# Kernel optimization log

Measured on AMD Instinct MI355X. Metric: run time of the kernel, lower is better.

## Reference

```python
import jax, jax.numpy as jnp
import numpy as np

B, D, N = 128, 2, 8192
C_CENT, K, R = 32, 32, 0.25
BOTTLE = 8
BN_EPS = 1e-5


def setup_inputs() -> dict:
    key = jax.random.key(0)
    ks = jax.random.split(key, 12)
    w = lambda k, s: jax.random.normal(k, s, dtype=jnp.float32) * 0.05
    z = lambda s: jnp.zeros(s, jnp.float32)
    o = lambda s: jnp.ones(s, jnp.float32)
    return {
        "x": jax.random.normal(ks[0], (B, D, N), dtype=jnp.float32),
        "eps": jax.random.normal(ks[1], (B, BOTTLE), dtype=jnp.float32),
        "sa_c1_w": w(ks[2], (64, D)), "sa_c1_b": z((64,)),
        "sa_bn1_g": o((64,)), "sa_bn1_b": z((64,)),
        "sa_c2_w": w(ks[3], (128, 64)), "sa_c2_b": z((128,)),
        "sa_bn2_g": o((128,)), "sa_bn2_b": z((128,)),
        "sa_c3_w": w(ks[4], (256, 128)), "sa_c3_b": z((256,)),
        "sa_bn3_g": o((256,)), "sa_bn3_b": z((256,)),
        "sa_fc1_w": w(ks[5], (1024, 256 * C_CENT)), "sa_fc1_b": z((1024,)),
        "sa_bn4_g": o((1024,)), "sa_bn4_b": z((1024,)),
        "sa_fc2_w": w(ks[6], (256, 1024)), "sa_fc2_b": z((256,)),
        "sa_bn5_g": o((256,)), "sa_bn5_b": z((256,)),
        "sa_fc3_w": w(ks[7], (BOTTLE, 256)), "sa_fc3_b": z((BOTTLE,)),
        "fce1_w": w(ks[8], (BOTTLE, BOTTLE)), "fce1_b": z((BOTTLE,)),
        "fce2_w": w(ks[9], (BOTTLE, BOTTLE)), "fce2_b": z((BOTTLE,)),
        "dfc1_w": w(ks[10], (32, BOTTLE)), "dfc1_b": z((32,)),
        "dfc2_w": w(ks[11], (128, 32)), "dfc2_b": z((128,)),
        "dfc3_w": w(jax.random.fold_in(key, 99), (512, 128)), "dfc3_b": z((512,)),
    }


def _bn2d(x, g, b):
    m = jnp.mean(x, axis=(0, 2, 3), keepdims=True)
    v = jnp.var(x, axis=(0, 2, 3), keepdims=True)
    return (x - m) * jax.lax.rsqrt(v + BN_EPS) * g[None, :, None, None] + b[None, :, None, None]


def _bn1d(x, g, b):
    m = jnp.mean(x, axis=0, keepdims=True)
    v = jnp.var(x, axis=0, keepdims=True)
    return (x - m) * jax.lax.rsqrt(v + BN_EPS) * g[None, :] + b[None, :]


def _fps(points, n_centroids):
    # points: [B, D, N]; deterministic start at index 0 (torch uses randint)
    c0 = points[:, :, 0]                                   # [B, D]
    dist0 = jnp.sum((c0[:, :, None] - points) ** 2, axis=1)  # [B, N]

    def step(dist, _):
        ind = jnp.argmax(dist, axis=1)                      # [B]
        c = jnp.take_along_axis(points, ind[:, None, None], axis=2)[:, :, 0]  # [B, D]
        dist = jnp.minimum(dist, jnp.sum((c[:, :, None] - points) ** 2, axis=1))
        return dist, c

    _, cs = jax.lax.scan(step, dist0, None, length=n_centroids - 1)  # [C-1, B, D]
    cents = jnp.concatenate([c0[None], cs], axis=0)          # [C, B, D]
    return jnp.transpose(cents, (1, 2, 0))                   # [B, D, C]


def _group_points(points):
    b, _, n = points.shape
    cents = _fps(points, C_CENT)                             # [B, D, C]
    # squared pairwise distances centroid->point: [B, C, N]
    sq = (-2.0 * jnp.einsum('bdc,bdn->bcn', cents, points)
          + jnp.sum(cents ** 2, axis=1)[:, :, None]
          + jnp.sum(points ** 2, axis=1)[:, None, :])
    idx = jnp.broadcast_to(jnp.arange(n, dtype=jnp.int32), (b, C_CENT, n))
    idx = jnp.where(sq > R * R, jnp.int32(n), idx)
    idx = jnp.sort(idx, axis=-1)[:, :, :K]                   # [B, C, K]
    first = idx[:, :, :1]
    idx = jnp.where(idx == n, first, idx)
    bidx = jnp.arange(b)[:, None, None]
    grouped = points[bidx, :, idx]                            # [B, C, K, D]
    return jnp.transpose(grouped, (0, 3, 1, 2))               # [B, D, C, K]


def reference(x, eps, sa_c1_w, sa_c1_b, sa_bn1_g, sa_bn1_b, sa_c2_w, sa_c2_b,
              sa_bn2_g, sa_bn2_b, sa_c3_w, sa_c3_b, sa_bn3_g, sa_bn3_b,
              sa_fc1_w, sa_fc1_b, sa_bn4_g, sa_bn4_b, sa_fc2_w, sa_fc2_b,
              sa_bn5_g, sa_bn5_b, sa_fc3_w, sa_fc3_b, fce1_w, fce1_b,
              fce2_w, fce2_b, dfc1_w, dfc1_b, dfc2_w, dfc2_b, dfc3_w, dfc3_b):
    b = x.shape[0]
    g = _group_points(x)                                     # [B, D, C, K]
    h = jax.nn.relu(_bn2d(jnp.einsum('bdck,od->bock', g, sa_c1_w) + sa_c1_b[None, :, None, None], sa_bn1_g, sa_bn1_b))
    h = jax.nn.relu(_bn2d(jnp.einsum('bdck,od->bock', h, sa_c2_w) + sa_c2_b[None, :, None, None], sa_bn2_g, sa_bn2_b))
    h = jax.nn.relu(_bn2d(jnp.einsum('bdck,od->bock', h, sa_c3_w) + sa_c3_b[None, :, None, None], sa_bn3_g, sa_bn3_b))
    h = jnp.max(h, axis=3)                                   # [B, 256, C]
    h = h.reshape(b, 256 * C_CENT)
    h = jax.nn.relu(_bn1d(h @ sa_fc1_w.T + sa_fc1_b, sa_bn4_g, sa_bn4_b))
    h = jax.nn.relu(_bn1d(h @ sa_fc2_w.T + sa_fc2_b, sa_bn5_g, sa_bn5_b))
    feat = jax.nn.relu(h @ sa_fc3_w.T + sa_fc3_b)            # [B, 8]
    mu = feat @ fce1_w.T + fce1_b
    logvar = feat @ fce2_w.T + fce2_b
    zlat = eps * jnp.exp(0.5 * logvar) + mu                  # reparametrize
    d = jax.nn.relu(zlat @ dfc1_w.T + dfc1_b)
    d = jax.nn.relu(d @ dfc2_w.T + dfc2_b)
    d = d @ dfc3_w.T + dfc3_b
    out = d.reshape(-1, 2, 256)
    return out, mu, logvar
```

## Files before the change

### kernel.cpp

```cpp
#include <hip/hip_runtime.h>
#include <cstdint>
#include <cstddef>

#define NB   128
#define NPT  8192
#define NC   32
#define NK   32
#define MSP  131072
#define R2   0.0625f

typedef unsigned short u16;
typedef unsigned long long u64;
typedef __attribute__((ext_vector_type(8))) short short8v;
typedef __attribute__((ext_vector_type(4))) float f32x4;

static constexpr size_t OFF_CENTS  = 0;
static constexpr size_t OFF_GX     = 8192;
static constexpr size_t OFF_GY     = OFF_GX + 131072;
static constexpr size_t OFF_H1Q    = OFF_GY + 131072;
static constexpr size_t OFF_H2Q    = OFF_H1Q + 4194304;
static constexpr size_t OFF_MAXPRE = OFF_H1Q;
static constexpr size_t OFF_P3S    = OFF_H1Q + 1048576;
static constexpr size_t OFF_P3Q    = OFF_H1Q + 2097152;
static constexpr size_t OFF_PART1  = OFF_H2Q;
static constexpr size_t OFF_PART2  = OFF_H2Q + 4194304;
static constexpr size_t OFF_FC1    = OFF_H2Q + 8388608;
static constexpr size_t OFF_FC2    = OFF_FC1 + 131072;
static constexpr size_t OFF_W2Q    = OFF_FC2 + 32768;
static constexpr size_t OFF_W3Q    = OFF_W2Q + 4096;
static constexpr size_t OFF_PMOM   = OFF_W3Q + 16384;
static constexpr size_t OFF_P2S    = OFF_PMOM + 20480;
static constexpr size_t OFF_P2Q    = OFF_P2S + 131072;
static constexpr size_t OFF_SC1    = OFF_P2Q + 131072;
static constexpr size_t OFF_SH1    = OFF_SC1 + 64;
static constexpr size_t OFF_SC2    = OFF_SH1 + 64;
static constexpr size_t OFF_SH2    = OFF_SC2 + 128;
static constexpr size_t OFF_SC3    = OFF_SH2 + 128;
static constexpr size_t OFF_SH3    = OFF_SC3 + 256;
static constexpr size_t OFF_SC4    = OFF_SH3 + 256;
static constexpr size_t OFF_SH4    = OFF_SC4 + 1024;
static constexpr size_t OFF_SC5    = OFF_SH4 + 1024;
static constexpr size_t OFF_SH5    = OFF_SC5 + 256;
static constexpr size_t OFF_SC3E   = OFF_SH5 + 256;
static constexpr size_t OFF_SH3E   = OFF_SC3E + 8192;

__device__ __forceinline__ u16 f2bf(float f) {
  uint32_t u = __float_as_uint(f);
  u += 0x7FFFu + ((u >> 16) & 1u);
  return (u16)(u >> 16);
}
__device__ __forceinline__ float bf2f(u16 h) {
  return __uint_as_float(((uint32_t)h) << 16);
}
__device__ __forceinline__ void gload16(const void* g, void* l) {
  __builtin_amdgcn_global_load_lds(
      (const __attribute__((address_space(1))) void*)g,
      (__attribute__((address_space(3))) void*)l, 16, 0, 0);
}

__global__ __launch_bounds__(512) void fps_kernel(const float* __restrict__ x,
                                                  float* __restrict__ cents,
                                                  const float* __restrict__ c2w,
                                                  const float* __restrict__ c3w,
                                                  u16* __restrict__ w2q,
                                                  u16* __restrict__ w3qf) {
  const int b = blockIdx.x, t = threadIdx.x;
  const int lane = t & 63, wid = t >> 6;

  if (b < 12) {
    const int id = b * 512 + t;
    if (id < 2048) {
      const int e = id * 4;
      const float4 v = *(const float4*)(c2w + e);
      uint2 q;
      q.x = (uint32_t)f2bf(v.x) | ((uint32_t)f2bf(v.y) << 16);
      q.y = (uint32_t)f2bf(v.z) | ((uint32_t)f2bf(v.w) << 16);
      *(uint2*)(w2q + e) = q;
    } else {
      const int id2 = id - 2048;
      const int oc = id2 >> 4, k8 = (id2 & 15) * 8;
      const float4 v0 = *(const float4*)(c3w + oc * 128 + k8);
      const float4 v1 = *(const float4*)(c3w + oc * 128 + k8 + 4);
      uint4 q;
      q.x = (uint32_t)f2bf(v0.x) | ((uint32_t)f2bf(v0.y) << 16);
      q.y = (uint32_t)f2bf(v0.z) | ((uint32_t)f2bf(v0.w) << 16);
      q.z = (uint32_t)f2bf(v1.x) | ((uint32_t)f2bf(v1.y) << 16);
      q.w = (uint32_t)f2bf(v1.z) | ((uint32_t)f2bf(v1.w) << 16);
      const int off = ((((oc >> 4) * 4 + (k8 >> 5)) * 4 + ((k8 & 31) >> 3)) * 16 + (oc & 15)) * 8;
      *(uint4*)(w3qf + off) = q;
    }
  }

  const float* xb = x + (size_t)b * 2 * NPT;
  float px[16], py[16], dst[16];
  __shared__ float lpx[NPT], lpy[NPT];
  __shared__ u64 slot[2][8];
  __shared__ float cxs[NC], cys[NC];
#pragma unroll
  for (int k = 0; k < 16; k++) {
    const int id = t + k * 512;
    px[k] = xb[id];
    py[k] = xb[NPT + id];
    lpx[id] = px[k];
    lpy[id] = py[k];
  }
  const float c0x = xb[0], c0y = xb[NPT];
  if (t == 0) { cxs[0] = c0x; cys[0] = c0y; }
  float bm = -1.0f;
  int bi = 0;
#pragma unroll
  for (int k = 0; k < 16; k++) {
    const float dx = __fsub_rn(c0x, px[k]);
    const float dy = __fsub_rn(c0y, py[k]);
    dst[k] = __fadd_rn(__fmul_rn(dx, dx), __fmul_rn(dy, dy));
    if (dst[k] > bm) { bm = dst[k]; bi = t + k * 512; }
  }
  u64 best = ((u64)__float_as_uint(bm) << 32) | (uint32_t)~(uint32_t)bi;
  __syncthreads();
  for (int j = 1; j < NC; j++) {
#pragma unroll
    for (int off = 1; off < 64; off <<= 1) {
      const u64 o = __shfl_xor(best, off);
      if (o > best) best = o;
    }
    const int pb = j & 1;
    if (lane == 0) slot[pb][wid] = best;
    __syncthreads();
    u64 w = slot[pb][0];
#pragma unroll
    for (int s = 1; s < 8; s++) {
      const u64 o = slot[pb][s];
      if (o > w) w = o;
    }
    const int wi = (int)~(uint32_t)w;
    const float wx = lpx[wi], wy = lpy[wi];
    if (t == 0) { cxs[j] = wx; cys[j] = wy; }
    bm = -1.0f;
    bi = 0;
#pragma unroll
    for (int k = 0; k < 16; k++) {
      const float dx = __fsub_rn(wx, px[k]);
      const float dy = __fsub_rn(wy, py[k]);
      const float nd = __fadd_rn(__fmul_rn(dx, dx), __fmul_rn(dy, dy));
      dst[k] = fminf(dst[k], nd);
      if (dst[k] > bm) { bm = dst[k]; bi = t + k * 512; }
    }
    best = ((u64)__float_as_uint(bm) << 32) | (uint32_t)~(uint32_t)bi;
  }
  __syncthreads();
  if (t < NC) {
    cents[(size_t)b * 64 + t]      = cxs[t];
    cents[(size_t)b * 64 + 32 + t] = cys[t];
  }
}

__global__ __launch_bounds__(512) void group_kernel(const float* __restrict__ x,
                                                    const float* __restrict__ cents,
                                                    float* __restrict__ gx,
                                                    float* __restrict__ gy,
                                                    float* __restrict__ pmom) {
  const int b  = blockIdx.x & 127;
  const int cg = blockIdx.x >> 7;
  const int t = threadIdx.x;
  const int lane = t & 63, wid = t >> 6;
  const float* px = x + (size_t)b * 2 * NPT;
  const float* py = px + NPT;
  const int p0 = t * 16;

  float lx[16], ly[16], sp[16];
#pragma unroll
  for (int k = 0; k < 16; k += 4) {
    const float4 vx = *(const float4*)(px + p0 + k);
    const float4 vy = *(const float4*)(py + p0 + k);
    lx[k] = vx.x; lx[k + 1] = vx.y; lx[k + 2] = vx.z; lx[k + 3] = vx.w;
    ly[k] = vy.x; ly[k + 1] = vy.y; ly[k + 2] = vy.z; ly[k + 3] = vy.w;
  }
#pragma unroll
  for (int k = 0; k < 16; k++)
    sp[k] = __fadd_rn(__fmul_rn(lx[k], lx[k]), __fmul_rn(ly[k], ly[k]));

  __shared__ int idxs[8][NK];
  __shared__ int wtot[8][8];
  uint32_t mask[8];
  int ebase[8];

#pragma unroll
  for (int c = 0; c < 8; c++) {
    const int cc = cg * 8 + c;
    const float cx = cents[(size_t)b * 64 + cc];
    const float cy = cents[(size_t)b * 64 + 32 + cc];
    const float sc = __fadd_rn(__fmul_rn(cx, cx), __fmul_rn(cy, cy));
    uint32_t m = 0;
#pragma unroll
    for (int k = 0; k < 16; k++) {
      const float dot = __fadd_rn(__fmul_rn(cx, lx[k]), __fmul_rn(cy, ly[k]));
      const float sq  = __fadd_rn(__fadd_rn(__fmul_rn(-2.0f, dot), sc), sp[k]);
      if (!(sq > R2)) m |= (1u << k);
    }
    mask[c] = m;
    const int cnt = (int)__popc(m);
    int pre = cnt;
#pragma unroll
    for (int off = 1; off < 64; off <<= 1) {
      const int o = __shfl_up(pre, off);
      if (lane >= off) pre += o;
    }
    ebase[c] = pre - cnt;
    if (lane == 63) wtot[c][wid] = pre;
  }
  __syncthreads();
#pragma unroll
  for (int c = 0; c < 8; c++) {
    int off = 0;
#pragma unroll
    for (int w = 0; w < 8; w++) off += (w < wid) ? wtot[c][w] : 0;
    int pos = ebase[c] + off;
    uint32_t m = mask[c];
    while (m && pos < NK) {
      const int k = __ffs(m) - 1;
      idxs[c][pos] = p0 + k;
      m &= m - 1;
      pos++;
    }
  }
  __syncthreads();
  {
    int tot = 0;
#pragma unroll
    for (int w = 0; w < 8; w++) tot += wtot[wid][w];
    if (lane >= tot && lane < NK) idxs[wid][lane] = idxs[wid][0];
  }
  __syncthreads();
  {
    const int bc = b * 32 + cg * 8 + wid;
    float gxv = 0.f, gyv = 0.f;
    if (lane < NK) {
      const int id = idxs[wid][lane];
      gxv = px[id];
      gyv = py[id];
      const size_t s = (size_t)bc * NK + lane;
      gx[s] = gxv;
      gy[s] = gyv;
    }
    float sx = gxv, sy = gyv;
    float sxx = gxv * gxv, syy = gyv * gyv, sxy = gxv * gyv;
#pragma unroll
    for (int off = 1; off < 64; off <<= 1) {
      sx  += __shfl_xor(sx, off);
      sy  += __shfl_xor(sy, off);
      sxx += __shfl_xor(sxx, off);
      syy += __shfl_xor(syy, off);
      sxy += __shfl_xor(sxy, off);
    }
    if (lane == 0) {
      pmom[0 * 4096 + bc] = sx;
      pmom[1 * 4096 + bc] = sy;
      pmom[2 * 4096 + bc] = sxx;
      pmom[3 * 4096 + bc] = syy;
      pmom[4 * 4096 + bc] = sxy;
    }
  }
}

__global__ __launch_bounds__(256) void bn1fin_kernel(const float* __restrict__ pmom,
                                                     const float* __restrict__ w,
                                                     const float* __restrict__ gamma,
                                                     const float* __restrict__ beta,
                                                     float* __restrict__ sc,
                                                     float* __restrict__ sh) {
  const int t = threadIdx.x, lane = t & 63, wid = t >> 6;
  __shared__ float rr[5][4];
  __shared__ float red[5];
#pragma unroll
  for (int m = 0; m < 5; m++) {
    float a = 0.f;
#pragma unroll
    for (int i = 0; i < 4; i++) {
      const float4 v = *(const float4*)(pmom + m * 4096 + (t + i * 256) * 4);
      a += v.x + v.y + v.z + v.w;
    }
#pragma unroll
    for (int off = 1; off < 64; off <<= 1) a += __shfl_xor(a, off);
    if (lane == 0) rr[m][wid] = a;
  }
  __syncthreads();
  if (t == 0) {
#pragma unroll
    for (int m = 0; m < 5; m++) red[m] = rr[m][0] + rr[m][1] + rr[m][2] + rr[m][3];
  }
  __syncthreads();
  if (t < 64) {
    const double invM = 1.0 / (double)MSP;
    const double mx = red[0] * invM, my = red[1] * invM;
    const double exx = red[2] * invM, eyy = red[3] * invM, exy = red[4] * invM;
    const double w0 = w[2 * t], w1 = w[2 * t + 1];
    const double mean = w0 * mx + w1 * my;
    double var = w0 * w0 * (exx - mx * mx) + 2.0 * w0 * w1 * (exy - mx * my)
               + w1 * w1 * (eyy - my * my);
    if (var < 0.0) var = 0.0;
    const double s = (double)gamma[t] / sqrt(var + 1e-5);
    sc[t] = (float)s;
    sh[t] = (float)((double)beta[t] - mean * s);
  }
}

__global__ __launch_bounds__(256) void finalize_kernel(
    const float* __restrict__ psum, const float* __restrict__ psq,
    int P, float invM,
    const float* __restrict__ gamma, const float* __restrict__ beta,
    float* __restrict__ scale, float* __restrict__ shift,
    float* __restrict__ scexp, float* __restrict__ shexp, int expand) {
  const int c = blockIdx.x, t = threadIdx.x;
  float s = 0.f, q = 0.f;
  for (int p = t; p < P; p += 256) {
    s += psum[(size_t)c * P + p];
    q += psq[(size_t)c * P + p];
  }
#pragma unroll
  for (int off = 1; off < 64; off <<= 1) {
    s += __shfl_xor(s, off);
    q += __shfl_xor(q, off);
  }
  __shared__ float r1[4], r2[4], bc2[2];
  if ((t & 63) == 0) { r1[t >> 6] = s; r2[t >> 6] = q; }
  __syncthreads();
  if (t == 0) {
    s = r1[0] + r1[1] + r1[2] + r1[3];
    q = r2[0] + r2[1] + r2[2] + r2[3];
    const float m = s * invM;
    float v = fmaf(-m, m, q * invM);
    v = fmaxf(v, 0.f);
    const float sc = gamma[c] * (float)(1.0 / sqrt((double)v + 1e-5));
    const float sh = fmaf(-m, sc, beta[c]);
    scale[c] = sc;
    shift[c] = sh;
    bc2[0] = sc;
    bc2[1] = sh;
  }
  __syncthreads();
  if (t < expand) {
    scexp[c * expand + t] = bc2[0];
    shexp[c * expand + t] = bc2[1];
  }
}

__global__ __launch_bounds__(256) void bncol_kernel(
    const float* __restrict__ in, int rows, int cols,
    const float* __restrict__ gamma, const float* __restrict__ beta,
    float* __restrict__ scale, float* __restrict__ shift) {
  const int jl = threadIdx.x & 63;
  const int rg = threadIdx.x >> 6;
  const int j = blockIdx.x * 64 + jl;
  float s = 0.f, q = 0.f;
  for (int r = rg; r < rows; r += 4) {
    const float v = in[(size_t)r * cols + j];
    s += v;
    q = fmaf(v, v, q);
  }
  __shared__ float rs[4][64], rq[4][64];
  rs[rg][jl] = s;
  rq[rg][jl] = q;
  __syncthreads();
  if (rg == 0) {
    s = rs[0][jl] + rs[1][jl] + rs[2][jl] + rs[3][jl];
    q = rq[0][jl] + rq[1][jl] + rq[2][jl] + rq[3][jl];
    const float m = s / (float)rows;
    float var = q / (float)rows - m * m;
    var = fmaxf(var, 0.f);
    const float sc = gamma[j] * (float)(1.0 / sqrt((double)var + 1e-5));
    scale[j] = sc;
    shift[j] = fmaf(-m, sc, beta[j]);
  }
}

__global__ __launch_bounds__(512) void conv2fused_kernel(
    const float* __restrict__ gx, const float* __restrict__ gy,
    const float* __restrict__ w1,
    const float* __restrict__ sc1, const float* __restrict__ sh1,
    const u16* __restrict__ wq,
    u16* __restrict__ outq,
    float* __restrict__ psum, float* __restrict__ psq) {
  constexpr int K = 64, OCB = 128, BS = 128, OCT = 128;
  constexpr int RB = K * 2;
  constexpr int STAGE = (OCB + BS) * RB;
  constexpr int EPI = BS * OCB * 2 + 4 * OCB * 2 * 4;
  constexpr int SMEM = STAGE > EPI ? STAGE : EPI;
  __shared__ __align__(16) char smem[SMEM + 1024];
  char* Wl = smem;
  char* Bl = smem + OCB * RB;
  float* par = (float*)(smem + SMEM);
  const int t = threadIdx.x;
  const int lane = t & 63, wid = t >> 6;
  const int sblk = blockIdx.x;
  const int s_base = sblk * BS;

  if (t < 64) {
    par[t]       = w1[t * 2];
    par[64 + t]  = w1[t * 2 + 1];
    par[128 + t] = sc1[t];
    par[192 + t] = sh1[t];
  }
  __syncthreads();

  {
    constexpr int CH = OCB * RB / 16, PW = CH / 8, NI = PW / 64;
#pragma unroll
    for (int j = 0; j < NI; j++) {
      const int c = wid * PW + j * 64 + lane;
      const int b = c * 16;
      const int oc = b / RB;
      const int off = b & (RB - 1);
      gload16((const char*)wq + (size_t)oc * RB + (off ^ ((oc & 7) << 4)),
              Wl + (wid * PW + j * 64) * 16);
    }
  }
  {
    const int sl = t >> 2;
    const int cq = t & 3;
    const float xx = gx[s_base + sl], yy = gy[s_base + sl];
    uint32_t pk[8];
#pragma unroll
    for (int h = 0; h < 8; h++) {
      const int c = cq * 16 + 2 * h;
      float v0 = fmaf(par[c],     xx, par[64 + c]     * yy);
      float v1 = fmaf(par[c + 1], xx, par[64 + c + 1] * yy);
      v0 = fmaxf(fmaf(v0, par[128 + c],     par[192 + c]),     0.f);
      v1 = fmaxf(fmaf(v1, par[128 + c + 1], par[192 + c + 1]), 0.f);
      pk[h] = (uint32_t)f2bf(v0) | ((uint32_t)f2bf(v1) << 16);
    }
    *(uint4*)(Bl + sl * RB + ((cq * 32)      ^ ((sl & 7) << 4))) = *(uint4*)&pk[0];
    *(uint4*)(Bl + sl * RB + ((cq * 32 + 16) ^ ((sl & 7) << 4))) = *(uint4*)&pk[4];
  }
  __syncthreads();

  const int wr = wid >> 2, wc = wid & 3;
  const int l15 = lane & 15, l4 = lane >> 4;
  f32x4 acc[4][2];
#pragma unroll
  for (int fo = 0; fo < 4; fo++)
#pragma unroll
    for (int fs = 0; fs < 2; fs++)
#pragma unroll
      for (int q = 0; q < 4; q++) acc[fo][fs][q] = 0.f;

#pragma unroll
  for (int ks = 0; ks < K / 32; ks++) {
    short8v a[4], bv[2];
#pragma unroll
    for (int f = 0; f < 4; f++) {
      const int oc = wr * 64 + f * 16 + l15;
      a[f] = *(const short8v*)(Wl + oc * RB + ((ks * 64 + l4 * 16) ^ ((oc & 7) << 4)));
    }
#pragma unroll
    for (int f = 0; f < 2; f++) {
      const int sl = wc * 32 + f * 16 + l15;
      bv[f] = *(const short8v*)(Bl + sl * RB + ((ks * 64 + l4 * 16) ^ ((sl & 7) << 4)));
    }
#pragma unroll
    for (int fo = 0; fo < 4; fo++)
#pragma unroll
      for (int fs = 0; fs < 2; fs++)
        acc[fo][fs] = __builtin_amdgcn_mfma_f32_16x16x32_bf16(a[fo], bv[fs], acc[fo][fs], 0, 0, 0);
  }
  __syncthreads();

  char* Dl = smem;
  float* sred1 = (float*)(smem + BS * OCB * 2);
  float* sred2 = sred1 + 4 * OCB;

#pragma unroll
  for (int fo = 0; fo < 4; fo++)
#pragma unroll
    for (int r = 0; r < 4; r++) {
      float s1 = acc[fo][0][r] + acc[fo][1][r];
      float s2 = fmaf(acc[fo][0][r], acc[fo][0][r], acc[fo][1][r] * acc[fo][1][r]);
#pragma unroll
      for (int off = 1; off < 16; off <<= 1) {
        s1 += __shfl_xor(s1, off);
        s2 += __shfl_xor(s2, off);
      }
      if (l15 == 0) {
        const int ocl = wr * 64 + fo * 16 + l4 * 4 + r;
        sred1[wc * OCB + ocl] = s1;
        sred2[wc * OCB + ocl] = s2;
      }
    }

#pragma unroll
  for (int fo = 0; fo < 4; fo++)
#pragma unroll
    for (int fs = 0; fs < 2; fs++) {
      const int sl = wc * 32 + fs * 16 + l15;
      const int ocl = wr * 64 + fo * 16 + l4 * 4;
      uint2 q;
      q.x = (uint32_t)f2bf(acc[fo][fs][0]) | ((uint32_t)f2bf(acc[fo][fs][1]) << 16);
      q.y = (uint32_t)f2bf(acc[fo][fs][2]) | ((uint32_t)f2bf(acc[fo][fs][3]) << 16);
      *(uint2*)(Dl + sl * 256 + ((ocl * 2) ^ ((sl & 7) << 4))) = q;
    }
  __syncthreads();

  if (t < OCB) {
    psum[(size_t)t * 1024 + sblk] =
        sred1[t] + sred1[OCB + t] + sred1[2 * OCB + t] + sred1[3 * OCB + t];
    psq[(size_t)t * 1024 + sblk] =
        sred2[t] + sred2[OCB + t] + sred2[2 * OCB + t] + sred2[3 * OCB + t];
  }
#pragma unroll
  for (int i = 0; i < 4; i++) {
    const int c = t + i * 512;
    const int sl = c >> 4, slot = c & 15;
    const uint4 v = *(const uint4*)(Dl + sl * 256 + ((slot * 16) ^ ((sl & 7) << 4)));
    *(uint4*)(outq + (size_t)(s_base + sl) * OCT + slot * 8) = v;
  }
}

__global__ __launch_bounds__(512) void conv3_kernel(
    const u16* __restrict__ act,
    const u16* __restrict__ wqf,
    const float* __restrict__ ascale, const float* __restrict__ ashift,
    float* __restrict__ psum, float* __restrict__ psq,
    float* __restrict__ maxpre) {
  constexpr int K = 128, RB = 256;
  __shared__ __align__(16) char Bl[64 * RB];
  const int t = threadIdx.x;
  const int lane = t & 63, wid = t >> 6;
  const int ws = wid & 1, wo = wid >> 1;
  const int sblk = blockIdx.x;
  const int l15 = lane & 15, l4 = lane >> 4;
  const int s_base = sblk * 64;

  short8v b[4][4];
  {
    const int ocq0 = wo * 4;
#pragma unroll
    for (int fo = 0; fo < 4; fo++)
#pragma unroll
      for (int ks = 0; ks < 4; ks++)
        b[fo][ks] = *(const short8v*)(wqf + ((((ocq0 + fo) * 4 + ks) * 4 + l4) * 16 + l15) * 8);
  }

  {
    const int kk0 = (t & 15) * 8;
    const float4 scA = *(const float4*)(ascale + kk0);
    const float4 scB = *(const float4*)(ascale + kk0 + 4);
    const float4 shA = *(const float4*)(ashift + kk0);
    const float4 shB = *(const float4*)(ashift + kk0 + 4);
    const float scr[8] = {scA.x, scA.y, scA.z, scA.w, scB.x, scB.y, scB.z, scB.w};
    const float shr[8] = {shA.x, shA.y, shA.z, shA.w, shB.x, shB.y, shB.z, shB.w};
#pragma unroll
    for (int i = 0; i < 2; i++) {
      const int sl = (t >> 4) + i * 32;
      const uint4 raw = *(const uint4*)(act + (size_t)(s_base + sl) * K + kk0);
      const u16* rp = (const u16*)&raw;
      uint32_t pk[4];
#pragma unroll
      for (int h = 0; h < 4; h++) {
        const float f0 = fmaxf(fmaf(bf2f(rp[2 * h]),     scr[2 * h],     shr[2 * h]),     0.f);
        const float f1 = fmaxf(fmaf(bf2f(rp[2 * h + 1]), scr[2 * h + 1], shr[2 * h + 1]), 0.f);
        pk[h] = (uint32_t)f2bf(f0) | ((uint32_t)f2bf(f1) << 16);
      }
      *(uint4*)(Bl + sl * RB + ((kk0 * 2) ^ ((sl & 7) << 4))) = *(uint4*)pk;
    }
  }
  __syncthreads();

  f32x4 acc[2][4];
#pragma unroll
  for (int fs = 0; fs < 2; fs++)
#pragma unroll
    for (int fo = 0; fo < 4; fo++)
#pragma unroll
      for (int q = 0; q < 4; q++) acc[fs][fo][q] = 0.f;

#pragma unroll
  for (int ks = 0; ks < 4; ks++) {
    short8v a[2];
#pragma unroll
    for (int fs = 0; fs < 2; fs++) {
      const int srow = ws * 32 + fs * 16 + l15;
      a[fs] = *(const short8v*)(Bl + srow * RB + ((ks * 64 + l4 * 16) ^ ((srow & 7) << 4)));
    }
#pragma unroll
    for (int fs = 0; fs < 2; fs++)
#pragma unroll
      for (int fo = 0; fo < 4; fo++)
        acc[fs][fo] = __builtin_amdgcn_mfma_f32_16x16x32_bf16(a[fs], b[fo][ks], acc[fs][fo], 0, 0, 0);
  }

  const int gid = sblk * 2 + ws;
#pragma unroll
  for (int fo = 0; fo < 4; fo++) {
    float s1 = acc[0][fo][0], s2 = acc[0][fo][0] * acc[0][fo][0];
    float mx = acc[0][fo][0];
#pragma unroll
    for (int fs = 0; fs < 2; fs++)
#pragma unroll
      for (int r = 0; r < 4; r++) {
        if (fs == 0 && r == 0) continue;
        const float v = acc[fs][fo][r];
        s1 += v;
        s2 = fmaf(v, v, s2);
        mx = fmaxf(mx, v);
      }
    s1 += __shfl_xor(s1, 16); s1 += __shfl_xor(s1, 32);
    s2 += __shfl_xor(s2, 16); s2 += __shfl_xor(s2, 32);
    mx = fmaxf(mx, __shfl_xor(mx, 16));
    mx = fmaxf(mx, __shfl_xor(mx, 32));
    if (l4 == 0) {
      const int oc = wo * 64 + fo * 16 + l15;
      psum[(size_t)oc * 4096 + gid] = s1;
      psq [(size_t)oc * 4096 + gid] = s2;
      maxpre[(size_t)oc * 4096 + gid] = mx;
    }
  }
}

template <int KL, bool TRANS, bool GATHER>
__global__ __launch_bounds__(512) void fcmfma_kernel(
    const float* __restrict__ A,
    const float* __restrict__ W,
    const float* __restrict__ ascale, const float* __restrict__ ashift,
    float* __restrict__ part,
    int Ntot, int Ktot) {
  __shared__ __align__(16) char smem[65536];
  char* Wh = smem;
  char* Wl = smem + 16384;
  char* Ah = smem + 32768;
  char* Al = smem + 49152;
  const int t = threadIdx.x;
  const int lane = t & 63, wid = t >> 6;
  const int sblk = blockIdx.x;
  const int n_base = blockIdx.y * 128;
  const int k_begin = sblk * KL;
  const int kq = t & 15;
  const int r0 = t >> 4;
  const int kk = kq * 4;
  const int wn = wid & 1, wm = wid >> 1;
  const int l15 = lane & 15, l4 = lane >> 4;

  f32x4 acc[4][2];
#pragma unroll
  for (int fo = 0; fo < 4; fo++)
#pragma unroll
    for (int fs = 0; fs < 2; fs++)
#pragma unroll
      for (int q = 0; q < 4; q++) acc[fo][fs][q] = 0.f;

  float4 wv[4], av[4], tsc, tsh;
  {
    const int kabs = k_begin + kk;
    if constexpr (TRANS) {
      tsc = *(const float4*)(ascale + kabs);
      tsh = *(const float4*)(ashift + kabs);
    }
#pragma unroll
    for (int i = 0; i < 4; i++) {
      const int row = r0 + i * 32;
      wv[i] = *(const float4*)(W + (size_t)(n_base + row) * Ktot + kabs);
      if constexpr (GATHER)
        av[i] = *(const float4*)(A + (size_t)(kabs >> 5) * 4096 + row * 32 + (kabs & 31));
      else
        av[i] = *(const float4*)(A + (size_t)row * Ktot + kabs);
    }
  }

  for (int c0 = 0; c0 < KL; c0 += 64) {
#pragma unroll
    for (int i = 0; i < 4; i++) {
      const int row = r0 + i * 32;
      const int byte = row * 128 + ((kk * 2) ^ ((row & 7) << 4));
      {
        const float4 v = wv[i];
        const u16 h0 = f2bf(v.x), h1 = f2bf(v.y), h2 = f2bf(v.z), h3 = f2bf(v.w);
        uint2 hv, lv;
        hv.x = (uint32_t)h0 | ((uint32_t)h1 << 16);
        hv.y = (uint32_t)h2 | ((uint32_t)h3 << 16);
        lv.x = (uint32_t)f2bf(v.x - bf2f(h0)) | ((uint32_t)f2bf(v.y - bf2f(h1)) << 16);
        lv.y = (uint32_t)f2bf(v.z - bf2f(h2)) | ((uint32_t)f2bf(v.w - bf2f(h3)) << 16);
        *(uint2*)(Wh + byte) = hv;
        *(uint2*)(Wl + byte) = lv;
      }
      {
        float4 v = av[i];
        if constexpr (TRANS) {
          v.x = fmaxf(fmaf(v.x, tsc.x, tsh.x), 0.f);
          v.y = fmaxf(fmaf(v.y, tsc.y, tsh.y), 0.f);
          v.z = fmaxf(fmaf(v.z, tsc.z, tsh.z), 0.f);
          v.w = fmaxf(fmaf(v.w, tsc.w, tsh.w), 0.f);
        }
        const u16 h0 = f2bf(v.x), h1 = f2bf(v.y), h2 = f2bf(v.z), h3 = f2bf(v.w);
        uint2 hv, lv;
        hv.x = (uint32_t)h0 | ((uint32_t)h1 << 16);
        hv.y = (uint32_t)h2 | ((uint32_t)h3 << 16);
        lv.x = (uint32_t)f2bf(v.x - bf2f(h0)) | ((uint32_t)f2bf(v.y - bf2f(h1)) << 16);
        lv.y = (uint32_t)f2bf(v.z - bf2f(h2)) | ((uint32_t)f2bf(v.w - bf2f(h3)) << 16);
        *(uint2*)(Ah + byte) = hv;
        *(uint2*)(Al + byte) = lv;
      }
    }
    __syncthreads();
    if (c0 + 64 < KL) {
      const int kabs = k_begin + c0 + 64 + kk;
      if constexpr (TRANS) {
        tsc = *(const float4*)(ascale + kabs);
        tsh = *(const float4*)(ashift + kabs);
      }
#pragma unroll
      for (int i = 0; i < 4; i++) {
        const int row = r0 + i * 32;
        wv[i] = *(const float4*)(W + (size_t)(n_base + row) * Ktot + kabs);
        if constexpr (GATHER)
          av[i] = *(const float4*)(A + (size_t)(kabs >> 5) * 4096 + row * 32 + (kabs & 31));
        else
          av[i] = *(const float4*)(A + (size_t)row * Ktot + kabs);
      }
    }
#pragma unroll
    for (int ks = 0; ks < 2; ks++) {
      short8v ah[4], al_[4], bh[2], bl[2];
#pragma unroll
      for (int f = 0; f < 4; f++) {
        const int r = wn * 64 + f * 16 + l15;
        const int byte = r * 128 + ((ks * 64 + l4 * 16) ^ ((r & 7) << 4));
        ah[f]  = *(const short8v*)(Wh + byte);
        al_[f] = *(const short8v*)(Wl + byte);
      }
#pragma unroll
      for (int f = 0; f < 2; f++) {
        const int r = wm * 32 + f * 16 + l15;
        const int byte = r * 128 + ((ks * 64 + l4 * 16) ^ ((r & 7) << 4));
        bh[f] = *(const short8v*)(Ah + byte);
        bl[f] = *(const short8v*)(Al + byte);
      }
#pragma unroll
      for (int fo = 0; fo < 4; fo++)
#pragma unroll
        for (int fs = 0; fs < 2; fs++) {
          acc[fo][fs] = __builtin_amdgcn_mfma_f32_16x16x32_bf16(ah[fo],  bh[fs], acc[fo][fs], 0, 0, 0);
          acc[fo][fs] = __builtin_amdgcn_mfma_f32_16x16x32_bf16(ah[fo],  bl[fs], acc[fo][fs], 0, 0, 0);
          acc[fo][fs] = __builtin_amdgcn_mfma_f32_16x16x32_bf16(al_[fo], bh[fs], acc[fo][fs], 0, 0, 0);
        }
    }
    __syncthreads();
  }
#pragma unroll
  for (int fo = 0; fo < 4; fo++) {
    const int n0 = n_base + wn * 64 + fo * 16 + l4 * 4;
#pragma unroll
    for (int fs = 0; fs < 2; fs++) {
      const int m = wm * 32 + fs * 16 + l15;
      *(float4*)(part + ((size_t)sblk * 128 + m) * Ntot + n0) =
          make_float4(acc[fo][fs][0], acc[fo][fs][1], acc[fo][fs][2], acc[fo][fs][3]);
    }
  }
}

__global__ __launch_bounds__(256) void fcreduce_kernel(const float* __restrict__ part,
                                                       float* __restrict__ out,
                                                       int total, int S) {
  const int id = blockIdx.x * 256 + threadIdx.x;
  if (id >= total) return;
  float s = 0.f;
  for (int p = 0; p < S; p++) s += part[(size_t)p * total + id];
  out[id] = s;
}

__global__ __launch_bounds__(256) void tail_kernel(
    const float* __restrict__ fc2raw, const float* __restrict__ scale5, const float* __restrict__ shift5,
    const float* __restrict__ w3, const float* __restrict__ b3,
    const float* __restrict__ e1w, const float* __restrict__ e1b,
    const float* __restrict__ e2w, const float* __restrict__ e2b,
    const float* __restrict__ eps,
    const float* __restrict__ d1w, const float* __restrict__ d1b,
    const float* __restrict__ d2w, const float* __restrict__ d2b,
    const float* __restrict__ d3w, const float* __restrict__ d3b,
    float* __restrict__ out) {
  const int b = blockIdx.x, t = threadIdx.x;
  __shared__ float h5[256], feat[8], z[8], d1[32], d2[128];
  {
    const float v = fc2raw[(size_t)b * 256 + t];
    h5[t] = fmaxf(fmaf(v, scale5[t], shift5[t]), 0.f);
  }
  __syncthreads();
  if (t < 64) {
    const int o = t >> 3, p = t & 7;
    const float* wr = w3 + o * 256 + p * 32;
    const float* hr = h5 + p * 32;
    float s = 0.f;
    for (int i = 0; i < 32; i++) s = fmaf(hr[i], wr[i], s);
    s += __shfl_xor(s, 1);
    s += __shfl_xor(s, 2);
    s += __shfl_xor(s, 4);
    if (p == 0) feat[o] = fmaxf(s + b3[o], 0.f);
  }
  __syncthreads();
  if (t < 8) {
    float mu = e1b[t], lv = e2b[t];
    for (int j = 0; j < 8; j++) {
      mu = fmaf(feat[j], e1w[t * 8 + j], mu);
      lv = fmaf(feat[j], e2w[t * 8 + j], lv);
    }
    out[65536 + b * 8 + t] = mu;
    out[66560 + b * 8 + t] = lv;
    z[t] = fmaf(eps[b * 8 + t], expf(0.5f * lv), mu);
  }
  __syncthreads();
  if (t < 32) {
    float s = d1b[t];
    for (int j = 0; j < 8; j++) s = fmaf(z[j], d1w[t * 8 + j], s);
    d1[t] = fmaxf(s, 0.f);
  }
  __syncthreads();
  if (t < 128) {
    float s = d2b[t];
    for (int j = 0; j < 32; j++) s = fmaf(d1[j], d2w[t * 32 + j], s);
    d2[t] = fmaxf(s, 0.f);
  }
  __syncthreads();
  for (int o = t; o < 512; o += 256) {
    float s = d3b[o];
    for (int j = 0; j < 128; j++) s = fmaf(d2[j], d3w[o * 128 + j], s);
    out[(size_t)b * 512 + o] = s;
  }
}

extern "C" void kernel_launch(void* const* d_in, const int* in_sizes, int n_in,
                              void* d_out, int out_size, void* d_ws, size_t ws_size,
                              hipStream_t stream) {
  const float* x    = (const float*)d_in[0];
  const float* eps  = (const float*)d_in[1];
  const float* c1w  = (const float*)d_in[2];
  const float* bn1g = (const float*)d_in[4];
  const float* bn1b = (const float*)d_in[5];
  const float* c2w  = (const float*)d_in[6];
  const float* bn2g = (const float*)d_in[8];
  const float* bn2b = (const float*)d_in[9];
  const float* c3w  = (const float*)d_in[10];
  const float* bn3g = (const float*)d_in[12];
  const float* bn3b = (const float*)d_in[13];
  const float* f1w  = (const float*)d_in[14];
  const float* bn4g = (const float*)d_in[16];
  const float* bn4b = (const float*)d_in[17];
  const float* f2w  = (const float*)d_in[18];
  const float* bn5g = (const float*)d_in[20];
  const float* bn5b = (const float*)d_in[21];
  const float* f3w  = (const float*)d_in[22];
  const float* f3b  = (const float*)d_in[23];
  const float* e1w  = (const float*)d_in[24];
  const float* e1b  = (const float*)d_in[25];
  const float* e2w  = (const float*)d_in[26];
  const float* e2b  = (const float*)d_in[27];
  const float* d1w  = (const float*)d_in[28];
  const float* d1b  = (const float*)d_in[29];
  const float* d2w  = (const float*)d_in[30];
  const float* d2b  = (const float*)d_in[31];
  const float* d3w  = (const float*)d_in[32];
  const float* d3b  = (const float*)d_in[33];

  float* ws = (float*)d_ws;
  float* cents  = ws + OFF_CENTS;
  float* gx     = ws + OFF_GX;
  float* gy     = ws + OFF_GY;
  u16*   h2q    = (u16*)(ws + OFF_H2Q);
  u16*   w2q    = (u16*)(ws + OFF_W2Q);
  u16*   w3qf   = (u16*)(ws + OFF_W3Q);
  float* pmom   = ws + OFF_PMOM;
  float* maxpre = ws + OFF_MAXPRE;
  float* part1  = ws + OFF_PART1;
  float* part2  = ws + OFF_PART2;
  float* fc1o   = ws + OFF_FC1;
  float* fc2o   = ws + OFF_FC2;
  float* p2s = ws + OFF_P2S, *p2q = ws + OFF_P2Q;
  float* p3s = ws + OFF_P3S, *p3q = ws + OFF_P3Q;
  float* sc1 = ws + OFF_SC1, *sh1 = ws + OFF_SH1;
  float* sc2 = ws + OFF_SC2, *sh2 = ws + OFF_SH2;
  float* sc3 = ws + OFF_SC3, *sh3 = ws + OFF_SH3;
  float* sc4 = ws + OFF_SC4, *sh4 = ws + OFF_SH4;
  float* sc5 = ws + OFF_SC5, *sh5 = ws + OFF_SH5;
  float* sc3e = ws + OFF_SC3E, *sh3e = ws + OFF_SH3E;

  fps_kernel<<<NB, 512, 0, stream>>>(x, cents, c2w, c3w, w2q, w3qf);
  group_kernel<<<512, 512, 0, stream>>>(x, cents, gx, gy, pmom);

  bn1fin_kernel<<<1, 256, 0, stream>>>(pmom, c1w, bn1g, bn1b, sc1, sh1);

  conv2fused_kernel<<<1024, 512, 0, stream>>>(gx, gy, c1w, sc1, sh1, w2q,
                                              h2q, p2s, p2q);
  finalize_kernel<<<128, 256, 0, stream>>>(p2s, p2q, 1024, 1.f / MSP, bn2g, bn2b,
                                           sc2, sh2, nullptr, nullptr, 0);

  conv3_kernel<<<2048, 512, 0, stream>>>(h2q, w3qf, sc2, sh2, p3s, p3q, maxpre);
  finalize_kernel<<<256, 256, 0, stream>>>(p3s, p3q, 4096, 1.f / MSP, bn3g, bn3b,
                                           sc3, sh3, sc3e, sh3e, 32);

  fcmfma_kernel<256, true, true><<<dim3(32, 8), 512, 0, stream>>>(
      maxpre, f1w, sc3e, sh3e, part1, 1024, 8192);
  fcreduce_kernel<<<512, 256, 0, stream>>>(part1, fc1o, 131072, 32);
  bncol_kernel<<<16, 256, 0, stream>>>(fc1o, 128, 1024, bn4g, bn4b, sc4, sh4);

  fcmfma_kernel<128, true, false><<<dim3(8, 2), 512, 0, stream>>>(
      fc1o, f2w, sc4, sh4, part2, 256, 1024);
  fcreduce_kernel<<<128, 256, 0, stream>>>(part2, fc2o, 32768, 8);
  bncol_kernel<<<4, 256, 0, stream>>>(fc2o, 128, 256, bn5g, bn5b, sc5, sh5);

  tail_kernel<<<NB, 256, 0, stream>>>(fc2o, sc5, sh5, f3w, f3b, e1w, e1b, e2w, e2b, eps,
                                      d1w, d1b, d2w, d2b, d3w, d3b, (float*)d_out);
}
```

Before: 188.8 us.

## Load FC weight fragments directly into registers, staging only activations in LDS

The FC MFMA kernel now has each wave own 16 output rows. Each lane loads its weight row segment from global memory straight into MFMA A-operand registers and converts it to bf16 hi/lo there, so only the activation tile goes through shared memory. This halves LDS footprint and write traffic, which may allow more resident blocks. In exchange, weight global loads are less coalesced: each lane reads two 32-byte pieces of a row. B fragments are also no longer reused across output tiles, so LDS reads per MFMA rise.

```diff
diff --git a/kernel.cpp b/kernel.cpp
--- a/kernel.cpp
+++ b/kernel.cpp
@@ -622,11 +622,9 @@
     const float* __restrict__ ascale, const float* __restrict__ ashift,
     float* __restrict__ part,
     int Ntot, int Ktot) {
-  __shared__ __align__(16) char smem[65536];
-  char* Wh = smem;
-  char* Wl = smem + 16384;
-  char* Ah = smem + 32768;
-  char* Al = smem + 49152;
+  __shared__ __align__(16) char smem[32768];
+  char* Ah = smem;
+  char* Al = smem + 16384;
   const int t = threadIdx.x;
   const int lane = t & 63, wid = t >> 6;
   const int sblk = blockIdx.x;
@@ -635,20 +633,24 @@
   const int kq = t & 15;
   const int r0 = t >> 4;
   const int kk = kq * 4;
-  const int wn = wid & 1, wm = wid >> 1;
   const int l15 = lane & 15, l4 = lane >> 4;
-
-  f32x4 acc[4][2];
-#pragma unroll
-  for (int fo = 0; fo < 4; fo++)
-#pragma unroll
-    for (int fs = 0; fs < 2; fs++)
-#pragma unroll
-      for (int q = 0; q < 4; q++) acc[fo][fs][q] = 0.f;
+  const float* wrow = W + (size_t)(n_base + wid * 16 + l15) * Ktot;
+
+  f32x4 acc[8];
+#pragma unroll
+  for (int fs = 0; fs < 8; fs++)
+#pragma unroll
+    for (int q = 0; q < 4; q++) acc[fs][q] = 0.f;
 
   float4 wv[4], av[4], tsc, tsh;
   {
-    const int kabs = k_begin + kk;
+    const int k0 = k_begin;
+#pragma unroll
+    for (int ks = 0; ks < 2; ks++) {
+      wv[ks * 2]     = *(const float4*)(wrow + k0 + ks * 32 + l4 * 8);
+      wv[ks * 2 + 1] = *(const float4*)(wrow + k0 + ks * 32 + l4 * 8 + 4);
+    }
+    const int kabs = k0 + kk;
     if constexpr (TRANS) {
       tsc = *(const float4*)(ascale + kabs);
       tsh = *(const float4*)(ashift + kabs);
@@ -656,7 +658,6 @@
 #pragma unroll
     for (int i = 0; i < 4; i++) {
       const int row = r0 + i * 32;
-      wv[i] = *(const float4*)(W + (size_t)(n_base + row) * Ktot + kabs);
       if constexpr (GATHER)
         av[i] = *(const float4*)(A + (size_t)(kabs >> 5) * 4096 + row * 32 + (kabs & 31));
       else
@@ -669,38 +670,45 @@
     for (int i = 0; i < 4; i++) {
       const int row = r0 + i * 32;
       const int byte = row * 128 + ((kk * 2) ^ ((row & 7) << 4));
-      {
-        const float4 v = wv[i];
-        const u16 h0 = f2bf(v.x), h1 = f2bf(v.y), h2 = f2bf(v.z), h3 = f2bf(v.w);
-        uint2 hv, lv;
-        hv.x = (uint32_t)h0 | ((uint32_t)h1 << 16);
-        hv.y = (uint32_t)h2 | ((uint32_t)h3 << 16);
-        lv.x = (uint32_t)f2bf(v.x - bf2f(h0)) | ((uint32_t)f2bf(v.y - bf2f(h1)) << 16);
-        lv.y = (uint32_t)f2bf(v.z - bf2f(h2)) | ((uint32_t)f2bf(v.w - bf2f(h3)) << 16);
-        *(uint2*)(Wh + byte) = hv;
-        *(uint2*)(Wl + byte) = lv;
-      }
-      {
-        float4 v = av[i];
-        if constexpr (TRANS) {
-          v.x = fmaxf(fmaf(v.x, tsc.x, tsh.x), 0.f);
-          v.y = fmaxf(fmaf(v.y, tsc.y, tsh.y), 0.f);
-          v.z = fmaxf(fmaf(v.z, tsc.z, tsh.z), 0.f);
-          v.w = fmaxf(fmaf(v.w, tsc.w, tsh.w), 0.f);
-        }
-        const u16 h0 = f2bf(v.x), h1 = f2bf(v.y), h2 = f2bf(v.z), h3 = f2bf(v.w);
-        uint2 hv, lv;
-        hv.x = (uint32_t)h0 | ((uint32_t)h1 << 16);
-        hv.y = (uint32_t)h2 | ((uint32_t)h3 << 16);
-        lv.x = (uint32_t)f2bf(v.x - bf2f(h0)) | ((uint32_t)f2bf(v.y - bf2f(h1)) << 16);
-        lv.y = (uint32_t)f2bf(v.z - bf2f(h2)) | ((uint32_t)f2bf(v.w - bf2f(h3)) << 16);
-        *(uint2*)(Ah + byte) = hv;
-        *(uint2*)(Al + byte) = lv;
+      float4 v = av[i];
+      if constexpr (TRANS) {
+        v.x = fmaxf(fmaf(v.x, tsc.x, tsh.x), 0.f);
+        v.y = fmaxf(fmaf(v.y, tsc.y, tsh.y), 0.f);
+        v.z = fmaxf(fmaf(v.z, tsc.z, tsh.z), 0.f);
+        v.w = fmaxf(fmaf(v.w, tsc.w, tsh.w), 0.f);
+      }
+      const u16 h0 = f2bf(v.x), h1 = f2bf(v.y), h2 = f2bf(v.z), h3 = f2bf(v.w);
+      uint2 hv, lv;
+      hv.x = (uint32_t)h0 | ((uint32_t)h1 << 16);
+      hv.y = (uint32_t)h2 | ((uint32_t)h3 << 16);
+      lv.x = (uint32_t)f2bf(v.x - bf2f(h0)) | ((uint32_t)f2bf(v.y - bf2f(h1)) << 16);
+      lv.y = (uint32_t)f2bf(v.z - bf2f(h2)) | ((uint32_t)f2bf(v.w - bf2f(h3)) << 16);
+      *(uint2*)(Ah + byte) = hv;
+      *(uint2*)(Al + byte) = lv;
+    }
+    short8v ah[2], al_[2];
+#pragma unroll
+    for (int ks = 0; ks < 2; ks++) {
+      const float vals[8] = {wv[ks * 2].x,     wv[ks * 2].y,
+                             wv[ks * 2].z,     wv[ks * 2].w,
+                             wv[ks * 2 + 1].x, wv[ks * 2 + 1].y,
+                             wv[ks * 2 + 1].z, wv[ks * 2 + 1].w};
+#pragma unroll
+      for (int i = 0; i < 8; i++) {
+        const u16 h = f2bf(vals[i]);
+        ah[ks][i]  = (short)h;
+        al_[ks][i] = (short)f2bf(vals[i] - bf2f(h));
       }
     }
     __syncthreads();
     if (c0 + 64 < KL) {
-      const int kabs = k_begin + c0 + 64 + kk;
+      const int k0 = k_begin + c0 + 64;
+#pragma unroll
+      for (int ks = 0; ks < 2; ks++) {
+        wv[ks * 2]     = *(const float4*)(wrow + k0 + ks * 32 + l4 * 8);
+        wv[ks * 2 + 1] = *(const float4*)(wrow + k0 + ks * 32 + l4 * 8 + 4);
+      }
+      const int kabs = k0 + kk;
       if constexpr (TRANS) {
         tsc = *(const float4*)(ascale + kabs);
         tsh = *(const float4*)(ashift + kabs);
@@ -708,7 +716,6 @@
 #pragma unroll
       for (int i = 0; i < 4; i++) {
         const int row = r0 + i * 32;
-        wv[i] = *(const float4*)(W + (size_t)(n_base + row) * Ktot + kabs);
         if constexpr (GATHER)
           av[i] = *(const float4*)(A + (size_t)(kabs >> 5) * 4096 + row * 32 + (kabs & 31));
         else
@@ -717,41 +724,25 @@
     }
 #pragma unroll
     for (int ks = 0; ks < 2; ks++) {
-      short8v ah[4], al_[4], bh[2], bl[2];
-#pragma unroll
-      for (int f = 0; f < 4; f++) {
-        const int r = wn * 64 + f * 16 + l15;
+#pragma unroll
+      for (int fs = 0; fs < 8; fs++) {
+        const int r = fs * 16 + l15;
         const int byte = r * 128 + ((ks * 64 + l4 * 16) ^ ((r & 7) << 4));
-        ah[f]  = *(const short8v*)(Wh + byte);
-        al_[f] = *(const short8v*)(Wl + byte);
-      }
-#pragma unroll
-      for (int f = 0; f < 2; f++) {
-        const int r = wm * 32 + f * 16 + l15;
-        const int byte = r * 128 + ((ks * 64 + l4 * 16) ^ ((r & 7) << 4));
-        bh[f] = *(const short8v*)(Ah + byte);
-        bl[f] = *(const short8v*)(Al + byte);
-      }
-#pragma unroll
-      for (int fo = 0; fo < 4; fo++)
-#pragma unroll
-        for (int fs = 0; fs < 2; fs++) {
-          acc[fo][fs] = __builtin_amdgcn_mfma_f32_16x16x32_bf16(ah[fo],  bh[fs], acc[fo][fs], 0, 0, 0);
-          acc[fo][fs] = __builtin_amdgcn_mfma_f32_16x16x32_bf16(ah[fo],  bl[fs], acc[fo][fs], 0, 0, 0);
-          acc[fo][fs] = __builtin_amdgcn_mfma_f32_16x16x32_bf16(al_[fo], bh[fs], acc[fo][fs], 0, 0, 0);
-        }
+        const short8v bh = *(const short8v*)(Ah + byte);
+        const short8v bl = *(const short8v*)(Al + byte);
+        acc[fs] = __builtin_amdgcn_mfma_f32_16x16x32_bf16(ah[ks],  bh, acc[fs], 0, 0, 0);
+        acc[fs] = __builtin_amdgcn_mfma_f32_16x16x32_bf16(ah[ks],  bl, acc[fs], 0, 0, 0);
+        acc[fs] = __builtin_amdgcn_mfma_f32_16x16x32_bf16(al_[ks], bh, acc[fs], 0, 0, 0);
+      }
     }
     __syncthreads();
   }
-#pragma unroll
-  for (int fo = 0; fo < 4; fo++) {
-    const int n0 = n_base + wn * 64 + fo * 16 + l4 * 4;
-#pragma unroll
-    for (int fs = 0; fs < 2; fs++) {
-      const int m = wm * 32 + fs * 16 + l15;
-      *(float4*)(part + ((size_t)sblk * 128 + m) * Ntot + n0) =
-          make_float4(acc[fo][fs][0], acc[fo][fs][1], acc[fo][fs][2], acc[fo][fs][3]);
-    }
+  const int n0 = n_base + wid * 16 + l4 * 4;
+#pragma unroll
+  for (int fs = 0; fs < 8; fs++) {
+    const int m = fs * 16 + l15;
+    *(float4*)(part + ((size_t)sblk * 128 + m) * Ntot + n0) =
+        make_float4(acc[fs][0], acc[fs][1], acc[fs][2], acc[fs][3]);
   }
 }
 
```

Result: no change. 189.2 us (median of 2 runs) (+0.2%).
